# Optimization experiments

Measured on AMD Instinct MI355X. Metric: run time of the kernel, lower is better.

## Reference

```python
import jax, jax.numpy as jnp
import numpy as np
from jax import lax

RADIUS = 51  # radius=50 bumped to odd in __init__
# cv2.getGaussianKernel(51, 0): sigma = 0.3*((ksize-1)*0.5 - 1) + 0.8 = 8.0
SIGMA = 0.3 * ((RADIUS - 1) * 0.5 - 1) + 0.8
WEIGHT = 0.5
THRESHOLD = 10.0


def _gaussian_kernel2d():
    x = np.arange(RADIUS, dtype=np.float64) - (RADIUS - 1) / 2.0
    g = np.exp(-(x ** 2) / (2.0 * SIGMA ** 2))
    g = g / g.sum()
    k2d = np.outer(g, g)
    return jnp.asarray(k2d, dtype=jnp.float32)


def filter2d(img, kernel):
    # img: (b, h, w, c); kernel: (k, k); reflect pad + depthwise conv, VALID
    k = kernel.shape[-1]
    c = img.shape[-1]
    p = k // 2
    imgp = jnp.pad(img, [(0, 0), (p, p), (p, p), (0, 0)], mode='reflect')
    kern = jnp.tile(kernel[:, :, None, None].astype(img.dtype), (1, 1, 1, c))  # HWIO, I=1
    return lax.conv_general_dilated(
        imgp, kern, window_strides=(1, 1), padding='VALID',
        dimension_numbers=('NHWC', 'HWIO', 'NHWC'), feature_group_count=c)


def setup_inputs() -> dict:
    key = jax.random.key(0)
    img = jax.random.uniform(key, (16, 512, 512, 3), dtype=jnp.float32)
    kernel = _gaussian_kernel2d()
    return {"img": img, "kernel": kernel}


def reference(img, kernel):
    blur = filter2d(img, kernel)
    residual = img - blur
    mask = (jnp.abs(residual) * 255.0 > THRESHOLD).astype(img.dtype)
    soft_mask = filter2d(mask, kernel)
    sharp = jnp.clip(img + WEIGHT * residual, 0.0, 1.0)
    return soft_mask * sharp + (1.0 - soft_mask) * img
```

## Files before the change

kernel.cpp:

```cpp
#include <hip/hip_runtime.h>
#include <hip/hip_fp16.h>

#define BB 16
#define HH 512
#define ROWLEN 1536
#define KK 51
#define RR 25

__device__ __forceinline__ int sq(int q) { return q ^ ((q >> 3) & 7); }

__global__ void k_weights(const float* __restrict__ k2d, float* __restrict__ g,
                          __half2* __restrict__ g2) {
    int i = threadIdx.x;
    if (i < KK) {
        float s = 0.f;
        for (int j = 0; j < KK; ++j) s += k2d[i * KK + j];
        g[i] = s;
        g2[i] = __float2half2_rn(s);
    }
}

#define PSTR 576
template<bool U8>
__global__ __launch_bounds__(512, 4) void k_hconv(const void* __restrict__ srcv,
                                                  __half* __restrict__ dst,
                                                  __half* __restrict__ imgh,
                                                  const float* __restrict__ gsrc) {
    __shared__ __align__(16) float pl[12 * PSTR];
    const int t = threadIdx.x;
    const int row0 = blockIdx.x * 4;

    float gw[KK];
    #pragma unroll
    for (int i = 0; i < KK; ++i) gw[i] = gsrc[i];

    const int r = t >> 7;
    const int l = t & 127;
    const size_t rb = (size_t)(row0 + r) * ROWLEN;

    {
        float f[12];
        if (U8) {
            const unsigned char* s8 = (const unsigned char*)srcv + rb + 12 * l;
            unsigned int ww[3];
            ww[0] = *(const unsigned int*)(s8);
            ww[1] = *(const unsigned int*)(s8 + 4);
            ww[2] = *(const unsigned int*)(s8 + 8);
            #pragma unroll
            for (int k = 0; k < 12; ++k)
                f[k] = (float)((ww[k >> 2] >> ((k & 3) * 8)) & 0xffu);
        } else {
            const float* sf = (const float*)srcv + rb + 12 * l;
            *(float4*)&f[0] = *(const float4*)(sf);
            *(float4*)&f[4] = *(const float4*)(sf + 4);
            *(float4*)&f[8] = *(const float4*)(sf + 8);
            union { __half h[12]; uint2 u2[3]; } pi;
            #pragma unroll
            for (int k = 0; k < 12; ++k) pi.h[k] = __float2half_rn(f[k]);
            uint2* ip = (uint2*)(imgh + rb + 12 * l);
            ip[0] = pi.u2[0]; ip[1] = pi.u2[1]; ip[2] = pi.u2[2];
        }
        const int q = sq(7 + l);
        #pragma unroll
        for (int c = 0; c < 3; ++c) {
            float4 o;
            o.x = f[c]; o.y = f[3 + c]; o.z = f[6 + c]; o.w = f[9 + c];
            *(float4*)&pl[(r * 3 + c) * PSTR + 4 * q] = o;
        }
    }
    __syncthreads();

    #pragma unroll
    for (int it = 0; it < 2; ++it) {
        const int item = t + it * 512;
        if (item < 600) {
            const int p = item / 50, k = item % 50;
            int ed, es;
            if (k < 25) { const int j = k + 1;  ed = 28 - j;  es = 28 + j; }
            else        { const int j = k - 24; ed = 539 + j; es = 539 - j; }
            float* pb = &pl[p * PSTR];
            pb[4 * sq(ed >> 2) + (ed & 3)] = pb[4 * sq(es >> 2) + (es & 3)];
        }
    }
    __syncthreads();

    float acc[3][4];
    #pragma unroll
    for (int c = 0; c < 3; ++c)
        #pragma unroll
        for (int a = 0; a < 4; ++a) acc[c][a] = 0.f;

    #pragma unroll
    for (int c = 0; c < 3; ++c) {
        const float* pb = &pl[(r * 3 + c) * PSTR];
        #pragma unroll
        for (int v = 0; v < 15; ++v) {
            const float4 v4 = *(const float4*)&pb[4 * sq(l + v)];
            #pragma unroll
            for (int mm = 0; mm < 4; ++mm) {
                const float val = (&v4.x)[mm];
                #pragma unroll
                for (int a = 0; a < 4; ++a) {
                    const int jj = 4 * v + mm - a - 3;
                    if (jj >= 0 && jj < KK) acc[c][a] += gw[jj] * val;
                }
            }
        }
    }

    union { __half h[12]; uint2 u2[3]; } pk;
    #pragma unroll
    for (int a = 0; a < 4; ++a)
        #pragma unroll
        for (int c = 0; c < 3; ++c) pk.h[3 * a + c] = __float2half_rn(acc[c][a]);
    uint2* dp = (uint2*)(dst + rb + 12 * l);
    dp[0] = pk.u2[0]; dp[1] = pk.u2[1]; dp[2] = pk.u2[2];
}

#define HC 128
#define VROWS 178
#define HSTR 72

template<int MODE>
__global__ __launch_bounds__(256) void k_vconv(const __half* __restrict__ src,
                                               const __half* __restrict__ imgh,
                                               __half* __restrict__ sharp16,
                                               float* __restrict__ outp,
                                               unsigned char* __restrict__ mask8,
                                               const __half2* __restrict__ g2src) {
    __shared__ __align__(16) __half tile[VROWS * HSTR];
    const int t  = threadIdx.x;
    const int cg = t & 7;
    const int rg = t >> 3;
    const int bid = blockIdx.x;
    const int wcB = bid % 24;
    const int hB  = (bid / 24) & 3;
    const int b   = bid / 96;
    const int wc0 = wcB * 64;
    const int h0  = hB * HC;

    __half2 gw2[KK];
    #pragma unroll
    for (int i = 0; i < KK; ++i) gw2[i] = g2src[i];

    const size_t imgbase = (size_t)b * HH * ROWLEN;

    #pragma unroll
    for (int i = 0; i < 6; ++i) {
        const int m = t + 256 * i;
        if (m < VROWS * 8) {
            const int r = m >> 3, cc = m & 7;
            int hs = h0 - RR + r;
            hs = hs < 0 ? -hs : hs;
            hs = hs > 511 ? 1022 - hs : hs;
            *(uint4*)&tile[r * HSTR + 8 * cc] =
                *(const uint4*)&src[imgbase + (size_t)hs * ROWLEN + wc0 + 8 * cc];
        }
    }
    __syncthreads();

    __half2 acc[4][4];
    const __half2 z2 = __float2half2_rn(0.f);
    #pragma unroll
    for (int a = 0; a < 4; ++a)
        #pragma unroll
        for (int p = 0; p < 4; ++p) acc[a][p] = z2;

    const __half* base = &tile[(rg * 4) * HSTR + 8 * cg];
    #pragma unroll
    for (int jj = 0; jj < 54; ++jj) {
        const uint4 raw = *(const uint4*)(base + jj * HSTR);
        union { uint4 u; __half2 h2[4]; } v; v.u = raw;
        #pragma unroll
        for (int a = 0; a < 4; ++a) {
            const int tap = jj - a;
            if (tap >= 0 && tap < KK) {
                acc[a][0] = __hfma2(gw2[tap], v.h2[0], acc[a][0]);
                acc[a][1] = __hfma2(gw2[tap], v.h2[1], acc[a][1]);
                acc[a][2] = __hfma2(gw2[tap], v.h2[2], acc[a][2]);
                acc[a][3] = __hfma2(gw2[tap], v.h2[3], acc[a][3]);
            }
        }
    }

    #pragma unroll
    for (int a = 0; a < 4; ++a) {
        const int hh = h0 + rg * 4 + a;
        const size_t idx = imgbase + (size_t)hh * ROWLEN + wc0 + 8 * cg;
        union { uint4 u; __half2 h2[4]; } xl;
        xl.u = *(const uint4*)&imgh[idx];
        float xv[8], bv[8];
        #pragma unroll
        for (int p = 0; p < 4; ++p) {
            const float2 xf = __half22float2(xl.h2[p]);
            const float2 bf = __half22float2(acc[a][p]);
            xv[2*p] = xf.x; xv[2*p+1] = xf.y;
            bv[2*p] = bf.x; bv[2*p+1] = bf.y;
        }
        if (MODE == 0) {
            union { __half h[8]; uint4 u; } sh;
            unsigned int mwlo = 0, mwhi = 0;
            #pragma unroll
            for (int m = 0; m < 8; ++m) {
                const float x = xv[m];
                const float res = x - bv[m];
                sh.h[m] = __float2half_rn(fminf(fmaxf(x + 0.5f * res, 0.f), 1.f));
                const unsigned int bit = (fabsf(res) * 255.0f > 10.0f) ? 1u : 0u;
                if (m < 4) mwlo |= bit << (8 * m); else mwhi |= bit << (8 * (m - 4));
            }
            *(uint4*)&sharp16[idx] = sh.u;
            uint2 mo; mo.x = mwlo; mo.y = mwhi;
            *(uint2*)&mask8[idx] = mo;
        } else {
            union { uint4 u; __half2 h2[4]; } sl;
            sl.u = *(const uint4*)&sharp16[idx];
            float4 o0, o1;
            float* op = &o0.x;
            float ov[8];
            #pragma unroll
            for (int p = 0; p < 4; ++p) {
                const float2 sf = __half22float2(sl.h2[p]);
                const float x0 = xv[2*p],   s0 = sf.x;
                const float x1 = xv[2*p+1], s1 = sf.y;
                ov[2*p]   = x0 + bv[2*p]   * (s0 - x0);
                ov[2*p+1] = x1 + bv[2*p+1] * (s1 - x1);
            }
            o0.x = ov[0]; o0.y = ov[1]; o0.z = ov[2]; o0.w = ov[3];
            o1.x = ov[4]; o1.y = ov[5]; o1.z = ov[6]; o1.w = ov[7];
            (void)op;
            *(float4*)&outp[idx]     = o0;
            *(float4*)&outp[idx + 4] = o1;
        }
    }
}

extern "C" void kernel_launch(void* const* d_in, const int* in_sizes, int n_in,
                              void* d_out, int out_size, void* d_ws, size_t ws_size,
                              hipStream_t stream) {
    (void)in_sizes; (void)n_in; (void)out_size; (void)ws_size;
    const float* img = (const float*)d_in[0];
    const float* k2d = (const float*)d_in[1];
    float* out = (float*)d_out;

    const size_t NPX = (size_t)BB * HH * ROWLEN;
    char* ws = (char*)d_ws;
    float* g = (float*)ws;
    __half2* g2 = (__half2*)(ws + 256);
    __half* tbuf = (__half*)(ws + 512);
    unsigned char* mask8 = (unsigned char*)(ws + 512 + NPX * 2);
    __half* sharp16 = (__half*)(ws + 512 + NPX * 2 + NPX);
    __half* imgh    = (__half*)(ws + 512 + NPX * 2 + NPX + NPX * 2);

    const int nhblk = BB * HH / 4;
    const int nvblk = BB * 4 * 24;

    k_weights<<<1, 64, 0, stream>>>(k2d, g, g2);
    k_hconv<false><<<nhblk, 512, 0, stream>>>((const void*)img, tbuf, imgh, g);
    k_vconv<0><<<nvblk, 256, 0, stream>>>(tbuf, imgh, sharp16, out, mask8, g2);
    k_hconv<true><<<nhblk, 512, 0, stream>>>((const void*)mask8, tbuf, imgh, g);
    k_vconv<1><<<nvblk, 256, 0, stream>>>(tbuf, imgh, sharp16, out, mask8, g2);
}
```

Baseline: 106.6 us.

## Compute horizontal blur in packed fp16 with two rows per thread

```diff
diff --git a/kernel.cpp b/kernel.cpp
--- a/kernel.cpp
+++ b/kernel.cpp
@@ -22,99 +22,132 @@
 
 #define PSTR 576
 template<bool U8>
-__global__ __launch_bounds__(512, 4) void k_hconv(const void* __restrict__ srcv,
+__global__ __launch_bounds__(256, 4) void k_hconv(const void* __restrict__ srcv,
                                                   __half* __restrict__ dst,
                                                   __half* __restrict__ imgh,
-                                                  const float* __restrict__ gsrc) {
-    __shared__ __align__(16) float pl[12 * PSTR];
+                                                  const __half2* __restrict__ g2src) {
+    __shared__ __align__(16) __half2 pl[6 * PSTR];
     const int t = threadIdx.x;
     const int row0 = blockIdx.x * 4;
 
-    float gw[KK];
-    #pragma unroll
-    for (int i = 0; i < KK; ++i) gw[i] = gsrc[i];
-
-    const int r = t >> 7;
-    const int l = t & 127;
-    const size_t rb = (size_t)(row0 + r) * ROWLEN;
+    __half2 gw2[KK];
+    #pragma unroll
+    for (int i = 0; i < KK; ++i) gw2[i] = g2src[i];
+
+    const int rp = t >> 7;
+    const int l  = t & 127;
+    const size_t rb0 = (size_t)(row0 + 2 * rp) * ROWLEN;
+    const size_t rb1 = rb0 + ROWLEN;
 
     {
-        float f[12];
+        float f0[12], f1[12];
         if (U8) {
-            const unsigned char* s8 = (const unsigned char*)srcv + rb + 12 * l;
-            unsigned int ww[3];
-            ww[0] = *(const unsigned int*)(s8);
-            ww[1] = *(const unsigned int*)(s8 + 4);
-            ww[2] = *(const unsigned int*)(s8 + 8);
-            #pragma unroll
-            for (int k = 0; k < 12; ++k)
-                f[k] = (float)((ww[k >> 2] >> ((k & 3) * 8)) & 0xffu);
+            const unsigned char* sa = (const unsigned char*)srcv + rb0 + 12 * l;
+            const unsigned char* sb = (const unsigned char*)srcv + rb1 + 12 * l;
+            unsigned int wa[3], wb[3];
+            wa[0] = *(const unsigned int*)(sa);
+            wa[1] = *(const unsigned int*)(sa + 4);
+            wa[2] = *(const unsigned int*)(sa + 8);
+            wb[0] = *(const unsigned int*)(sb);
+            wb[1] = *(const unsigned int*)(sb + 4);
+            wb[2] = *(const unsigned int*)(sb + 8);
+            #pragma unroll
+            for (int k = 0; k < 12; ++k) {
+                f0[k] = (float)((wa[k >> 2] >> ((k & 3) * 8)) & 0xffu);
+                f1[k] = (float)((wb[k >> 2] >> ((k & 3) * 8)) & 0xffu);
+            }
         } else {
-            const float* sf = (const float*)srcv + rb + 12 * l;
-            *(float4*)&f[0] = *(const float4*)(sf);
-            *(float4*)&f[4] = *(const float4*)(sf + 4);
-            *(float4*)&f[8] = *(const float4*)(sf + 8);
-            union { __half h[12]; uint2 u2[3]; } pi;
-            #pragma unroll
-            for (int k = 0; k < 12; ++k) pi.h[k] = __float2half_rn(f[k]);
-            uint2* ip = (uint2*)(imgh + rb + 12 * l);
-            ip[0] = pi.u2[0]; ip[1] = pi.u2[1]; ip[2] = pi.u2[2];
+            const float* sfa = (const float*)srcv + rb0 + 12 * l;
+            const float* sfb = (const float*)srcv + rb1 + 12 * l;
+            *(float4*)&f0[0] = *(const float4*)(sfa);
+            *(float4*)&f0[4] = *(const float4*)(sfa + 4);
+            *(float4*)&f0[8] = *(const float4*)(sfa + 8);
+            *(float4*)&f1[0] = *(const float4*)(sfb);
+            *(float4*)&f1[4] = *(const float4*)(sfb + 4);
+            *(float4*)&f1[8] = *(const float4*)(sfb + 8);
+            union { __half h[12]; uint2 u2[3]; } pa, pb2;
+            #pragma unroll
+            for (int k = 0; k < 12; ++k) {
+                pa.h[k]  = __float2half_rn(f0[k]);
+                pb2.h[k] = __float2half_rn(f1[k]);
+            }
+            uint2* ipa = (uint2*)(imgh + rb0 + 12 * l);
+            uint2* ipb = (uint2*)(imgh + rb1 + 12 * l);
+            ipa[0] = pa.u2[0];  ipa[1] = pa.u2[1];  ipa[2] = pa.u2[2];
+            ipb[0] = pb2.u2[0]; ipb[1] = pb2.u2[1]; ipb[2] = pb2.u2[2];
         }
         const int q = sq(7 + l);
         #pragma unroll
         for (int c = 0; c < 3; ++c) {
-            float4 o;
-            o.x = f[c]; o.y = f[3 + c]; o.z = f[6 + c]; o.w = f[9 + c];
-            *(float4*)&pl[(r * 3 + c) * PSTR + 4 * q] = o;
+            union { __half2 h2[4]; uint4 u; } o;
+            #pragma unroll
+            for (int i = 0; i < 4; ++i)
+                o.h2[i] = __halves2half2(__float2half_rn(f0[3 * i + c]),
+                                         __float2half_rn(f1[3 * i + c]));
+            *(uint4*)&pl[(rp * 3 + c) * PSTR + 4 * q] = o.u;
         }
     }
     __syncthreads();
 
     #pragma unroll
     for (int it = 0; it < 2; ++it) {
-        const int item = t + it * 512;
-        if (item < 600) {
+        const int item = t + it * 256;
+        if (item < 300) {
             const int p = item / 50, k = item % 50;
             int ed, es;
             if (k < 25) { const int j = k + 1;  ed = 28 - j;  es = 28 + j; }
             else        { const int j = k - 24; ed = 539 + j; es = 539 - j; }
-            float* pb = &pl[p * PSTR];
+            __half2* pb = &pl[p * PSTR];
             pb[4 * sq(ed >> 2) + (ed & 3)] = pb[4 * sq(es >> 2) + (es & 3)];
         }
     }
     __syncthreads();
 
-    float acc[3][4];
+    __half2 acc2[3][4];
+    const __half2 z2 = __float2half2_rn(0.f);
     #pragma unroll
     for (int c = 0; c < 3; ++c)
         #pragma unroll
-        for (int a = 0; a < 4; ++a) acc[c][a] = 0.f;
+        for (int a = 0; a < 4; ++a) acc2[c][a] = z2;
 
     #pragma unroll
     for (int c = 0; c < 3; ++c) {
-        const float* pb = &pl[(r * 3 + c) * PSTR];
+        const __half2* pb = &pl[(rp * 3 + c) * PSTR];
         #pragma unroll
         for (int v = 0; v < 15; ++v) {
-            const float4 v4 = *(const float4*)&pb[4 * sq(l + v)];
+            union { uint4 u; __half2 h2[4]; } v4;
+            v4.u = *(const uint4*)&pb[4 * sq(l + v)];
             #pragma unroll
             for (int mm = 0; mm < 4; ++mm) {
-                const float val = (&v4.x)[mm];
+                const __half2 val = v4.h2[mm];
                 #pragma unroll
                 for (int a = 0; a < 4; ++a) {
                     const int jj = 4 * v + mm - a - 3;
-                    if (jj >= 0 && jj < KK) acc[c][a] += gw[jj] * val;
+                    if (jj >= 0 && jj < KK)
+                        acc2[c][a] = __hfma2(gw2[jj], val, acc2[c][a]);
                 }
             }
         }
     }
 
-    union { __half h[12]; uint2 u2[3]; } pk;
-    #pragma unroll
-    for (int a = 0; a < 4; ++a)
-        #pragma unroll
-        for (int c = 0; c < 3; ++c) pk.h[3 * a + c] = __float2half_rn(acc[c][a]);
-    uint2* dp = (uint2*)(dst + rb + 12 * l);
-    dp[0] = pk.u2[0]; dp[1] = pk.u2[1]; dp[2] = pk.u2[2];
+    {
+        union { __half h[12]; uint2 u2[3]; } pk;
+        #pragma unroll
+        for (int a = 0; a < 4; ++a)
+            #pragma unroll
+            for (int c = 0; c < 3; ++c) pk.h[3 * a + c] = __low2half(acc2[c][a]);
+        uint2* dp = (uint2*)(dst + rb0 + 12 * l);
+        dp[0] = pk.u2[0]; dp[1] = pk.u2[1]; dp[2] = pk.u2[2];
+    }
+    {
+        union { __half h[12]; uint2 u2[3]; } pk;
+        #pragma unroll
+        for (int a = 0; a < 4; ++a)
+            #pragma unroll
+            for (int c = 0; c < 3; ++c) pk.h[3 * a + c] = __high2half(acc2[c][a]);
+        uint2* dp = (uint2*)(dst + rb1 + 12 * l);
+        dp[0] = pk.u2[0]; dp[1] = pk.u2[1]; dp[2] = pk.u2[2];
+    }
 }
 
 #define HC 128
@@ -214,20 +247,16 @@
         } else {
             union { uint4 u; __half2 h2[4]; } sl;
             sl.u = *(const uint4*)&sharp16[idx];
-            float4 o0, o1;
-            float* op = &o0.x;
             float ov[8];
             #pragma unroll
             for (int p = 0; p < 4; ++p) {
                 const float2 sf = __half22float2(sl.h2[p]);
-                const float x0 = xv[2*p],   s0 = sf.x;
-                const float x1 = xv[2*p+1], s1 = sf.y;
-                ov[2*p]   = x0 + bv[2*p]   * (s0 - x0);
-                ov[2*p+1] = x1 + bv[2*p+1] * (s1 - x1);
-            }
+                ov[2*p]   = xv[2*p]   + bv[2*p]   * (sf.x - xv[2*p]);
+                ov[2*p+1] = xv[2*p+1] + bv[2*p+1] * (sf.y - xv[2*p+1]);
+            }
+            float4 o0, o1;
             o0.x = ov[0]; o0.y = ov[1]; o0.z = ov[2]; o0.w = ov[3];
             o1.x = ov[4]; o1.y = ov[5]; o1.z = ov[6]; o1.w = ov[7];
-            (void)op;
             *(float4*)&outp[idx]     = o0;
             *(float4*)&outp[idx + 4] = o1;
         }
@@ -255,8 +284,8 @@
     const int nvblk = BB * 4 * 24;
 
     k_weights<<<1, 64, 0, stream>>>(k2d, g, g2);
-    k_hconv<false><<<nhblk, 512, 0, stream>>>((const void*)img, tbuf, imgh, g);
+    k_hconv<false><<<nhblk, 256, 0, stream>>>((const void*)img, tbuf, imgh, g2);
     k_vconv<0><<<nvblk, 256, 0, stream>>>(tbuf, imgh, sharp16, out, mask8, g2);
-    k_hconv<true><<<nhblk, 512, 0, stream>>>((const void*)mask8, tbuf, imgh, g);
+    k_hconv<true><<<nhblk, 256, 0, stream>>>((const void*)mask8, tbuf, imgh, g2);
     k_vconv<1><<<nvblk, 256, 0, stream>>>(tbuf, imgh, sharp16, out, mask8, g2);
 }
```

After: 95.91 us. -10.1%, faster.
